# Kernel tuning notes

Hardware: AMD Instinct MI355X
Metric: run time of the kernel (lower is better)

The kernel has to match this reference:

```python
import jax, jax.numpy as jnp
import numpy as np

B, N, CS, CZ, CH, H, PQ, PV = 1, 768, 384, 128, 16, 12, 4, 8
INF, EPS, LN_EPS = 1e5, 1e-8, 1e-5


def setup_inputs() -> dict:
    key = jax.random.key(0)
    ks = jax.random.split(key, 16)
    def nrm(k, shape, scale=0.02):
        return jax.random.normal(k, shape, dtype=jnp.float32) * scale
    return {
        "s": jax.random.normal(ks[0], (B, N, CS), jnp.float32),
        "z": jax.random.normal(ks[1], (B, N, N, CZ), jnp.float32),
        "r_rot": jax.random.normal(ks[2], (B, N, 5, 3, 3), jnp.float32),
        "r_trans": jax.random.normal(ks[3], (B, N, 5, 3), jnp.float32),
        "mask": jnp.ones((B, N, 5), jnp.float32),
        "wq": nrm(ks[4], (H * CH, CS)), "bq": jnp.zeros((H * CH,), jnp.float32),
        "wkv": nrm(ks[5], (2 * H * CH, CS)), "bkv": jnp.zeros((2 * H * CH,), jnp.float32),
        "wqp": nrm(ks[6], (H * PQ * 3, CS)), "bqp": jnp.zeros((H * PQ * 3,), jnp.float32),
        "wkvp": nrm(ks[7], (H * (PQ + PV) * 3, CS)), "bkvp": jnp.zeros((H * (PQ + PV) * 3,), jnp.float32),
        "wb": nrm(ks[8], (H, CZ)), "bb": jnp.zeros((H,), jnp.float32),
        "head_w": nrm(ks[9], (H,), 0.5),
        "wout": nrm(ks[10], (CS, H * (CZ + CH + PV * 4))), "bout": jnp.zeros((CS,), jnp.float32),
        "wexp": nrm(ks[11], (5 * CS, CS)), "bexp": jnp.zeros((5 * CS,), jnp.float32),
        "ln_g": jnp.ones((CS,), jnp.float32), "ln_b": jnp.zeros((CS,), jnp.float32),
        "ww": nrm(ks[12], (1, CS)), "bw": jnp.zeros((1,), jnp.float32),
    }


def _mix(x, fg_mask, weight, ndims):
    # x: [B,N,5,...]; weighted blend of backbone frame (index 0) and mean of
    # masked functional-group frames (indices 1:5).
    bb_f = x[:, :, :1]
    m = fg_mask.reshape(fg_mask.shape + (1,) * ndims)
    fg = (x[:, :, 1:] * m).sum(axis=2, keepdims=True)
    denom = fg_mask.sum(-1, keepdims=True).reshape(fg_mask.shape[:2] + (1,) * (ndims + 1))
    fg = fg / (denom + 1e-8)
    w = weight.reshape(weight.shape[:2] + (1,) * (ndims + 1))
    return (w * bb_f + (1.0 - w) * fg)[:, :, 0]


def _ipa(s, z, r_rot, r_trans, mask, wq, bq, wkv, bkv, wqp, bqp, wkvp, bkvp,
         wb, bb, head_w, wout, bout, wexp, bexp, ln_g, ln_b, ww, bw):
    fg_mask = mask[..., 1:]            # [B,N,4]
    ulr = mask[..., 0]                 # [B,N]
    # softmax over a size-1 axis (as in original code -> all ones)
    weight = jax.nn.softmax(s @ ww.T + bw, axis=-1)   # [B,N,1]

    se = (s @ wexp.T + bexp).reshape(B, N, 5, CS)
    mu = se.mean(-1, keepdims=True)
    var = ((se - mu) ** 2).mean(-1, keepdims=True)
    se = (se - mu) * jax.lax.rsqrt(var + LN_EPS) * ln_g + ln_b

    q = _mix((se @ wq.T + bq).reshape(B, N, 5, H, CH), fg_mask, weight, 2)      # [B,N,H,CH]
    kv = _mix((se @ wkv.T + bkv).reshape(B, N, 5, H, 2 * CH), fg_mask, weight, 2)
    k, v = kv[..., :CH], kv[..., CH:]

    def pts_of(w_, b_, npts):
        lin = se @ w_.T + b_                                   # [B,N,5,3*H*npts]
        pts = jnp.moveaxis(lin.reshape(B, N, 5, 3, H * npts), -2, -1)  # [B,N,5,H*npts,3]
        pts = jnp.einsum('bnfij,bnfpj->bnfpi', r_rot, pts) + r_trans[:, :, :, None, :]
        return _mix(pts.reshape(B, N, 5, H, npts, 3), fg_mask, weight, 3)

    q_pts = pts_of(wqp, bqp, PQ)                               # [B,N,H,PQ,3]
    kv_pts = pts_of(wkvp, bkvp, PQ + PV)
    k_pts, v_pts = kv_pts[..., :PQ, :], kv_pts[..., PQ:, :]

    bias = z @ wb.T + bb                                       # [B,N,N,H]
    a = jnp.einsum('bihc,bjhc->bhij', q, k) * (1.0 / (3 * CH)) ** 0.5
    a = a + (1.0 / 3.0) ** 0.5 * jnp.transpose(bias, (0, 3, 1, 2))

    d2 = jnp.sum((q_pts[:, :, None] - k_pts[:, None]) ** 2, axis=-1)  # [B,N,N,H,PQ]
    hw = jax.nn.softplus(head_w) * (1.0 / (3 * (PQ * 9.0 / 2))) ** 0.5
    pt_att = -0.5 * jnp.sum(d2 * hw[:, None], axis=-1)         # [B,N,N,H]
    a = a + jnp.transpose(pt_att, (0, 3, 1, 2))
    sq_mask = INF * (ulr[:, :, None] * ulr[:, None, :] - 1.0)
    a = jax.nn.softmax(a + sq_mask[:, None], axis=-1)          # [B,H,N,N]

    o = jnp.einsum('bhij,bjhc->bihc', a, v).reshape(B, N, H * CH)
    o_pt = jnp.einsum('bhij,bjhpx->bihpx', a, v_pts)           # [B,N,H,PV,3]
    rot0, t0 = r_rot[:, :, 0], r_trans[:, :, 0]                # backbone frame
    # invert_apply: R^T (x - t)
    o_pt = jnp.einsum('bnik,bnhpi->bnhpk', rot0, o_pt - t0[:, :, None, None, :])
    o_pt_norm = jnp.sqrt(jnp.sum(o_pt ** 2, -1) + EPS).reshape(B, N, H * PV)
    o_pt = o_pt.reshape(B, N, H * PV, 3)
    o_pair = jnp.einsum('bhij,bijc->bihc', a, z).reshape(B, N, H * CZ)
    cat = jnp.concatenate([o, o_pt[..., 0], o_pt[..., 1], o_pt[..., 2], o_pt_norm, o_pair], -1)
    return cat @ wout.T + bout                                 # [B,N,CS]


def reference(s, z, r_rot, r_trans, mask, wq, bq, wkv, bkv, wqp, bqp, wkvp, bkvp,
              wb, bb, head_w, wout, bout, wexp, bexp, ln_g, ln_b, ww, bw):
    return _ipa(s, z, r_rot, r_trans, mask, wq, bq, wkv, bkv, wqp, bqp, wkvp, bkvp,
                wb, bb, head_w, wout, bout, wexp, bexp, ln_g, ln_b, ww, bw)
```

## Files before the change

### kernel.cpp

```cpp
#include <hip/hip_runtime.h>
#include <hip/hip_bf16.h>
#include <stdint.h>


typedef float  f32x4 __attribute__((ext_vector_type(4)));
typedef short  s16x8 __attribute__((ext_vector_type(8)));

__device__ __forceinline__ float bf2f(unsigned short u) {
    union { unsigned int i; float f; } v; v.i = ((unsigned int)u) << 16; return v.f;
}
__device__ __forceinline__ unsigned short f2bf(float f) {
    union { float f; unsigned int i; } v; v.f = f;
    unsigned int r = v.i + 0x7fffu + ((v.i >> 16) & 1u);
    return (unsigned short)(r >> 16);
}
__device__ __forceinline__ unsigned packbf2(float a, float b) {
    return (unsigned)f2bf(a) | ((unsigned)f2bf(b) << 16);
}
__device__ __forceinline__ float bval(int c,
    const float* bq, const float* bkv, const float* bqp, const float* bkvp)
{
    if (c < 192)      return bq[c];
    else if (c < 576) return bkv[c - 192];
    else if (c < 720) return bqp[c - 576];
    else              return bkvp[c - 720];
}

__global__ __launch_bounds__(256) void k_prep(
    const float* __restrict__ s, const float* __restrict__ wexp,
    const float* __restrict__ wq, const float* __restrict__ wkv,
    const float* __restrict__ wqp, const float* __restrict__ wkvp,
    const float* __restrict__ wout,
    const float* __restrict__ bq, const float* __restrict__ bkv,
    const float* __restrict__ bqp, const float* __restrict__ bkvp,
    unsigned short* __restrict__ s_bf, unsigned short* __restrict__ we_bf,
    unsigned short* __restrict__ wc_bf, unsigned short* __restrict__ wo_bf,
    float* __restrict__ bcat)
{
    const int x = blockIdx.x * 256 + threadIdx.x;
    if (x >= 1696896) return;
    if (x < 294912)            s_bf[x] = f2bf(s[x]);
    else if (x < 442368)       we_bf[x - 294912] = f2bf(wexp[x - 294912]);
    else if (x < 516096)       wc_bf[x - 442368] = f2bf(wq[x - 442368]);
    else if (x < 663552)       wc_bf[73728 + (x - 516096)] = f2bf(wkv[x - 516096]);
    else if (x < 718848)       wc_bf[221184 + (x - 663552)] = f2bf(wqp[x - 663552]);
    else if (x < 884736)       wc_bf[276480 + (x - 718848)] = f2bf(wkvp[x - 718848]);
    else if (x < 1695744)      wo_bf[x - 884736] = f2bf(wout[x - 884736]);
    else {
        int j = x - 1695744;
        bcat[j] = bval(j, bq, bkv, bqp, bkvp);
    }
}

__global__ __launch_bounds__(256) void k_mm(
    const unsigned short* __restrict__ A, int lda,
    const unsigned short* __restrict__ B, int ldb,
    float* __restrict__ C, int ldc, const float* __restrict__ bias,
    int nk, size_t pstride)
{
    const int m0 = blockIdx.x * 64, n0 = blockIdx.y * 64;
    const int koff = blockIdx.z * nk * 32;
    C += (size_t)blockIdx.z * pstride;
    const int t = threadIdx.x;
    const int lane = t & 63, wave = t >> 6, quad = lane >> 4, lcol = lane & 15;
    const int mh = (wave & 1) * 32, nh = (wave >> 1) * 32;
    __shared__ unsigned short As[64 * 40];
    __shared__ unsigned short Bs[64 * 40];
    const int lr = t >> 2, ls = (t & 3) * 8;
    const unsigned short* Ap = A + (size_t)(m0 + lr) * lda + koff + ls;
    const unsigned short* Bp = B + (size_t)(n0 + lr) * ldb + koff + ls;
    f32x4 acc[2][2] = {};

    uint4 av = *(const uint4*)Ap;
    uint4 bv = *(const uint4*)Bp;
    for (int kc = 0; kc < nk; ++kc) {
        __syncthreads();
        *(uint4*)&As[lr * 40 + ls] = av;
        *(uint4*)&Bs[lr * 40 + ls] = bv;
        __syncthreads();
        if (kc + 1 < nk) {
            av = *(const uint4*)(Ap + (size_t)(kc + 1) * 32);
            bv = *(const uint4*)(Bp + (size_t)(kc + 1) * 32);
        }
        s16x8 af0 = *(const s16x8*)&As[(mh + lcol) * 40 + quad * 8];
        s16x8 af1 = *(const s16x8*)&As[(mh + 16 + lcol) * 40 + quad * 8];
        s16x8 bf0 = *(const s16x8*)&Bs[(nh + lcol) * 40 + quad * 8];
        s16x8 bf1 = *(const s16x8*)&Bs[(nh + 16 + lcol) * 40 + quad * 8];
        acc[0][0] = __builtin_amdgcn_mfma_f32_16x16x32_bf16(af0, bf0, acc[0][0], 0, 0, 0);
        acc[0][1] = __builtin_amdgcn_mfma_f32_16x16x32_bf16(af0, bf1, acc[0][1], 0, 0, 0);
        acc[1][0] = __builtin_amdgcn_mfma_f32_16x16x32_bf16(af1, bf0, acc[1][0], 0, 0, 0);
        acc[1][1] = __builtin_amdgcn_mfma_f32_16x16x32_bf16(af1, bf1, acc[1][1], 0, 0, 0);
    }
    #pragma unroll
    for (int r = 0; r < 2; ++r)
        #pragma unroll
        for (int c = 0; c < 2; ++c) {
            int gn = n0 + nh + c * 16 + lcol;
            float bv2 = bias ? bias[gn] : 0.f;
            #pragma unroll
            for (int ii = 0; ii < 4; ++ii) {
                int gm = m0 + mh + r * 16 + quad * 4 + ii;
                C[(size_t)gm * ldc + gn] = acc[r][c][ii] + bv2;
            }
        }
}

__global__ __launch_bounds__(256) void k_ln(
    const float* __restrict__ se_raw, const float* __restrict__ ln_g,
    const float* __restrict__ ln_b, unsigned short* __restrict__ se0_bf)
{
    const int n = blockIdx.x * 4 + (threadIdx.x >> 6);
    const int lane = threadIdx.x & 63;
    const float* row = se_raw + (size_t)n * 384;
    float v[6], s1 = 0.f, s2 = 0.f;
    #pragma unroll
    for (int q = 0; q < 6; ++q) {
        v[q] = row[lane + q * 64];
        s1 += v[q]; s2 += v[q] * v[q];
    }
    for (int mk = 1; mk < 64; mk <<= 1) {
        s1 += __shfl_xor(s1, mk, 64);
        s2 += __shfl_xor(s2, mk, 64);
    }
    float mu = s1 * (1.f / 384.f);
    float var = s2 * (1.f / 384.f) - mu * mu;
    float rs = rsqrtf(fmaxf(var, 0.f) + 1e-5f);
    unsigned short* orow = se0_bf + (size_t)n * 384;
    #pragma unroll
    for (int q = 0; q < 6; ++q) {
        int c = lane + q * 64;
        orow[c] = f2bf((v[q] - mu) * rs * ln_g[c] + ln_b[c]);
    }
}

__global__ __launch_bounds__(256) void k_post(
    const float* __restrict__ lin,
    const float* __restrict__ r_rot, const float* __restrict__ r_trans,
    float* __restrict__ q_out, unsigned short* __restrict__ k_out,
    float* __restrict__ v_out, float* __restrict__ qp_out,
    unsigned short* __restrict__ kp_out, float* __restrict__ vp_out,
    float* __restrict__ k2_out)
{
    const int n0 = blockIdx.x * 8;
    const int t = threadIdx.x;
    __shared__ float kprot[8 * 144];

    for (int r = 0; r < 8; ++r) {
        const int n = n0 + r;
        const float* lrow = lin + (size_t)n * 1152;
        const float* rot = r_rot + (size_t)n * 45;
        for (int u = t; u < 1152; u += 256) {
            if (u < 192) {
                q_out[(size_t)n * 192 + u] = lrow[u];
            } else if (u < 576) {
                int l2 = u - 192, h = l2 >> 5, c = l2 & 31;
                float v = lrow[u];
                if (c < 16) k_out[(size_t)n * 192 + h * 16 + c] = f2bf(v);
                else        v_out[(size_t)n * 192 + h * 16 + (c - 16)] = v;
            } else {
                int y = u - 576;
                int pt = y / 3, i = y - pt * 3;
                float t0 = r_trans[(size_t)n * 15 + i];
                float v;
                if (pt < 48) {
                    v = rot[i*3+0] * lrow[576 + pt]
                      + rot[i*3+1] * lrow[576 + 48 + pt]
                      + rot[i*3+2] * lrow[576 + 96 + pt] + t0;
                    qp_out[(size_t)n * 144 + pt * 3 + i] = v;
                } else {
                    int pp = pt - 48;
                    v = rot[i*3+0] * lrow[720 + pp]
                      + rot[i*3+1] * lrow[720 + 144 + pp]
                      + rot[i*3+2] * lrow[720 + 288 + pp] + t0;
                    int h = pp / 12, pl = pp - h * 12;
                    if (pl < 4) {
                        kp_out[(size_t)n * 144 + (h * 4 + pl) * 3 + i] = f2bf(v);
                        kprot[r * 144 + (h * 4 + pl) * 3 + i] = v;
                    } else {
                        vp_out[(size_t)n * 288 + (h * 8 + (pl - 4)) * 3 + i] = v;
                    }
                }
            }
        }
    }
    __syncthreads();
    if (t < 96) {
        int r = t / 12, h = t - r * 12;
        float ss = 0.f;
        #pragma unroll
        for (int d = 0; d < 12; ++d) {
            float v = kprot[r * 144 + h * 12 + d];
            ss += v * v;
        }
        k2_out[(size_t)(n0 + r) * 12 + h] = ss;
    }
}

__global__ __launch_bounds__(256, 3) void k_attn(
    const float* __restrict__ z, const float* __restrict__ mask,
    const float* __restrict__ head_w, const float* __restrict__ wb,
    const float* __restrict__ bb,
    const float* __restrict__ r_rot, const float* __restrict__ r_trans,
    const float* __restrict__ q_ws, const float* __restrict__ qp_ws,
    const float* __restrict__ k2_ws,
    const unsigned short* __restrict__ k_bf, const float* __restrict__ v_f,
    const unsigned short* __restrict__ kp_bf, const float* __restrict__ vp_f,
    unsigned short* __restrict__ cat)
{
    const int i = blockIdx.x;
    const int t = threadIdx.x;
    const int lane = t & 63, wv = t >> 6;
    const int quad = lane >> 4, lcol = lane & 15;

    __shared__ short zb[2][64 * 136];
    __shared__ float L[64 * 17];
    __shared__ float Pt[16 * 68];
    __shared__ float qs[192], qps[144];
    __shared__ float ulra[768];
    __shared__ float m_s[16], l_s[16], alph_s[16], linv_s[16];
    __shared__ float optb[288];

    const float c_qk = 0.14433756729740643f;
    const float c_b  = 0.57735026918962576f;

    if (t < 192) qs[t]  = q_ws[(size_t)i * 192 + t];
    if (t < 144) qps[t] = qp_ws[(size_t)i * 144 + t];
    if (t >= 192 && t < 208) { int u = t - 192; m_s[u] = -1e30f; l_s[u] = 0.f; alph_s[u] = 1.f; }
    for (int x = t; x < 768; x += 256) ulra[x] = mask[(size_t)x * 5];
    for (int x = t; x < 4 * 68; x += 256) Pt[12 * 68 + x] = 0.f;
    const float ulr_i = mask[(size_t)i * 5];

    s16x8 wbf[4];
    #pragma unroll
    for (int kb = 0; kb < 4; ++kb) {
        #pragma unroll
        for (int j = 0; j < 8; ++j) {
            int c = kb * 32 + quad * 8 + j;
            wbf[kb][j] = (lcol < 12) ? (short)f2bf(wb[(size_t)lcol * 128 + c]) : (short)0;
        }
    }

    const int hh = (lcol < 12) ? lcol : 11;
    f32x4 qv[4], qpv[3];
    float q2_r = 0.f;
    {
        const float* qg  = q_ws  + (size_t)i * 192 + hh * 16;
        const float* qpg = qp_ws + (size_t)i * 144 + hh * 12;
        #pragma unroll
        for (int m = 0; m < 4; ++m) qv[m] = *(const f32x4*)(qg + m * 4);
        #pragma unroll
        for (int m = 0; m < 3; ++m) {
            qpv[m] = *(const f32x4*)(qpg + m * 4);
            #pragma unroll
            for (int e = 0; e < 4; ++e) q2_r += qpv[m][e] * qpv[m][e];
        }
    }
    float xh = head_w[hh];
    const float cpt_r = -0.5f * logf(1.f + __expf(xh)) * 0.13608276348795434f;
    const float cbb_r = c_b * bb[hh];

    f32x4 acc_op[2] = { {0.f,0.f,0.f,0.f}, {0.f,0.f,0.f,0.f} };
    f32x4 acc_s = {0.f,0.f,0.f,0.f};

    int vu = -1, vhalf = 0;
    if (t < 120) { vu = t; vhalf = 0; }
    else if (t >= 128 && t < 248) { vu = t - 128; vhalf = 1; }
    int vrole = -1; const float* vsrc = nullptr; int vstride = 0, voff = 0;
    if (vu >= 0) {
        if (vu < 48) { vrole = vu >> 2;       vsrc = v_f;  vstride = 192; voff = vu * 4; }
        else         { vrole = (vu - 48) / 6; vsrc = vp_f; vstride = 288; voff = (vu - 48) * 4; }
    }

    const int jlb = wv * 16 + quad * 4;
    const int zrow = wv * 16 + lcol;
    const int sigm = (zrow >> 3) & 3;

    const float* zbase = z + (size_t)i * 98304;
    f32x4 zr[8];
    #pragma unroll
    for (int sx = 0; sx < 8; ++sx)
        zr[sx] = *(const f32x4*)(zbase + (size_t)(t + sx * 256) * 4);
    #pragma unroll
    for (int sx = 0; sx < 8; ++sx) {
        int idx = t + sx * 256;
        int jl = idx >> 5, cq = idx & 31;
        int ch = (cq >> 1) ^ ((jl >> 3) & 3);
        uint2 pk;
        pk.x = packbf2(zr[sx][0], zr[sx][1]);
        pk.y = packbf2(zr[sx][2], zr[sx][3]);
        *(uint2*)&zb[0][jl * 136 + ch * 8 + (cq & 1) * 4] = pk;
    }
    #pragma unroll
    for (int sx = 0; sx < 8; ++sx)
        zr[sx] = *(const f32x4*)(zbase + 8192 + (size_t)(t + sx * 256) * 4);
    __syncthreads();

    int cur = 0;
    for (int tt = 0; tt < 12; ++tt) {
        const int j0 = tt * 64;

        uint4 ka[4], kb4[4]; uint2 p0[4], p1[4], p2[4]; float K2r[4];
        #pragma unroll
        for (int r = 0; r < 4; ++r) {
            int jr = j0 + jlb + r;
            const unsigned short* kr = k_bf + (size_t)jr * 192 + hh * 16;
            ka[r]  = *(const uint4*)kr;
            kb4[r] = *(const uint4*)(kr + 8);
            const unsigned short* pr = kp_bf + (size_t)jr * 144 + hh * 12;
            p0[r] = *(const uint2*)pr;
            p1[r] = *(const uint2*)(pr + 4);
            p2[r] = *(const uint2*)(pr + 8);
            K2r[r] = k2_ws[(size_t)jr * 12 + hh];
        }

        f32x4 d = {0.f, 0.f, 0.f, 0.f};
        #pragma unroll
        for (int kb = 0; kb < 4; ++kb) {
            s16x8 a = *(const s16x8*)&zb[cur][zrow * 136 + ((kb * 4 + quad) ^ sigm) * 8];
            d = __builtin_amdgcn_mfma_f32_16x16x32_bf16(a, wbf[kb], d, 0, 0, 0);
        }

        if (lcol < 12) {
            #pragma unroll
            for (int r = 0; r < 4; ++r) {
                int jl = jlb + r;
                const unsigned* kwa = (const unsigned*)&ka[r];
                const unsigned* kwb = (const unsigned*)&kb4[r];
                float qk = 0.f;
                #pragma unroll
                for (int m = 0; m < 4; ++m) {
                    qk += qv[m >> 1][(m & 1) * 2 + 0] * bf2f((unsigned short)(kwa[m] & 0xffffu));
                    qk += qv[m >> 1][(m & 1) * 2 + 1] * bf2f((unsigned short)(kwa[m] >> 16));
                }
                #pragma unroll
                for (int m = 0; m < 4; ++m) {
                    qk += qv[2 + (m >> 1)][(m & 1) * 2 + 0] * bf2f((unsigned short)(kwb[m] & 0xffffu));
                    qk += qv[2 + (m >> 1)][(m & 1) * 2 + 1] * bf2f((unsigned short)(kwb[m] >> 16));
                }
                float dp = 0.f;
                dp += qpv[0][0] * bf2f((unsigned short)(p0[r].x & 0xffffu));
                dp += qpv[0][1] * bf2f((unsigned short)(p0[r].x >> 16));
                dp += qpv[0][2] * bf2f((unsigned short)(p0[r].y & 0xffffu));
                dp += qpv[0][3] * bf2f((unsigned short)(p0[r].y >> 16));
                dp += qpv[1][0] * bf2f((unsigned short)(p1[r].x & 0xffffu));
                dp += qpv[1][1] * bf2f((unsigned short)(p1[r].x >> 16));
                dp += qpv[1][2] * bf2f((unsigned short)(p1[r].y & 0xffffu));
                dp += qpv[1][3] * bf2f((unsigned short)(p1[r].y >> 16));
                dp += qpv[2][0] * bf2f((unsigned short)(p2[r].x & 0xffffu));
                dp += qpv[2][1] * bf2f((unsigned short)(p2[r].x >> 16));
                dp += qpv[2][2] * bf2f((unsigned short)(p2[r].y & 0xffffu));
                dp += qpv[2][3] * bf2f((unsigned short)(p2[r].y >> 16));
                float ptt = cpt_r * (q2_r + K2r[r] - 2.f * dp);
                float lg = c_qk * qk + ptt + 1e5f * (ulr_i * ulra[j0 + jl] - 1.f)
                         + c_b * d[r] + cbb_r;
                L[jl * 17 + lcol] = lg;
            }
        }
        __syncthreads();

        if (t < 192) {
            int h = t >> 4, u = t & 15;
            float v0 = L[(u * 4 + 0) * 17 + h];
            float v1 = L[(u * 4 + 1) * 17 + h];
            float v2 = L[(u * 4 + 2) * 17 + h];
            float v3 = L[(u * 4 + 3) * 17 + h];
            float mx = fmaxf(fmaxf(v0, v1), fmaxf(v2, v3));
            for (int mk = 1; mk < 16; mk <<= 1) mx = fmaxf(mx, __shfl_xor(mx, mk, 16));
            float mold = m_s[h];
            float mnew = fmaxf(mold, mx);
            float w0 = __expf(v0 - mnew), w1 = __expf(v1 - mnew);
            float w2 = __expf(v2 - mnew), w3 = __expf(v3 - mnew);
            Pt[h * 68 + u * 4 + 0] = w0;
            Pt[h * 68 + u * 4 + 1] = w1;
            Pt[h * 68 + u * 4 + 2] = w2;
            Pt[h * 68 + u * 4 + 3] = w3;
            float sm = w0 + w1 + w2 + w3;
            for (int mk = 1; mk < 16; mk <<= 1) sm += __shfl_xor(sm, mk, 16);
            if (u == 0) {
                float al = __expf(mold - mnew);
                m_s[h] = mnew; alph_s[h] = al;
                l_s[h] = l_s[h] * al + sm;
            }
        }
        if (tt < 11) {
            #pragma unroll
            for (int sx = 0; sx < 8; ++sx) {
                int idx = t + sx * 256;
                int jl = idx >> 5, cq = idx & 31;
                int ch = (cq >> 1) ^ ((jl >> 3) & 3);
                uint2 pk;
                pk.x = packbf2(zr[sx][0], zr[sx][1]);
                pk.y = packbf2(zr[sx][2], zr[sx][3]);
                *(uint2*)&zb[cur ^ 1][jl * 136 + ch * 8 + (cq & 1) * 4] = pk;
            }
            if (tt < 10) {
                const float* znext = zbase + (size_t)(tt + 2) * 8192;
                #pragma unroll
                for (int sx = 0; sx < 8; ++sx)
                    zr[sx] = *(const f32x4*)(znext + (size_t)(t + sx * 256) * 4);
            }
        }
        __syncthreads();

        {
            float al[4];
            #pragma unroll
            for (int r = 0; r < 4; ++r) al[r] = alph_s[quad * 4 + r];
            #pragma unroll
            for (int nt = 0; nt < 2; ++nt)
                #pragma unroll
                for (int r = 0; r < 4; ++r) acc_op[nt][r] *= al[r];
            #pragma unroll
            for (int kb = 0; kb < 2; ++kb) {
                f32x4 pa = *(const f32x4*)&Pt[lcol * 68 + kb * 32 + quad * 8];
                f32x4 pb = *(const f32x4*)&Pt[lcol * 68 + kb * 32 + quad * 8 + 4];
                union { s16x8 v; unsigned u[4]; } af;
                af.u[0] = packbf2(pa[0], pa[1]);
                af.u[1] = packbf2(pa[2], pa[3]);
                af.u[2] = packbf2(pb[0], pb[1]);
                af.u[3] = packbf2(pb[2], pb[3]);
                #pragma unroll
                for (int nt = 0; nt < 2; ++nt) {
                    int c = wv * 32 + nt * 16 + lcol;
                    int csw = ((c >> 3) ^ quad) * 8 + (c & 7);
                    s16x8 bfg;
                    #pragma unroll
                    for (int j = 0; j < 8; ++j)
                        bfg[j] = zb[cur][(kb * 32 + quad * 8 + j) * 136 + csw];
                    acc_op[nt] = __builtin_amdgcn_mfma_f32_16x16x32_bf16(af.v, bfg, acc_op[nt], 0, 0, 0);
                }
            }
        }
        if (vu >= 0) {
            float alpha = alph_s[vrole];
            f32x4 a = acc_s;
            a[0] *= alpha; a[1] *= alpha; a[2] *= alpha; a[3] *= alpha;
            const float* prow = &Pt[vrole * 68 + vhalf * 32];
            const float* src = vsrc + (size_t)(j0 + vhalf * 32) * vstride + voff;
            #pragma unroll 4
            for (int jj = 0; jj < 32; jj += 4) {
                f32x4 p = *(const f32x4*)(prow + jj);
                #pragma unroll
                for (int m = 0; m < 4; ++m) {
                    f32x4 w = *(const f32x4*)(src + (size_t)(jj + m) * vstride);
                    float pm = p[m];
                    a[0] += pm * w[0];
                    a[1] += pm * w[1];
                    a[2] += pm * w[2];
                    a[3] += pm * w[3];
                }
            }
            acc_s = a;
        }
        if (tt < 11) cur ^= 1;
    }

    __syncthreads();
    if (t < 16) linv_s[t] = (t < 12) ? 1.f / l_s[t] : 0.f;
    float* vbuf = L;
    if (vu >= 0) {
        #pragma unroll
        for (int m = 0; m < 4; ++m) vbuf[(vu * 2 + vhalf) * 4 + m] = acc_s[m];
    }
    __syncthreads();
    unsigned short* crow = cat + (size_t)i * 2112;
    if (t < 120) {
        int role = (t < 48) ? (t >> 2) : (t - 48) / 6;
        float li = linv_s[role];
        float f[4];
        #pragma unroll
        for (int m = 0; m < 4; ++m)
            f[m] = (vbuf[(t * 2) * 4 + m] + vbuf[(t * 2 + 1) * 4 + m]) * li;
        if (t < 48) {
            #pragma unroll
            for (int m = 0; m < 4; ++m) crow[t * 4 + m] = f2bf(f[m]);
        } else {
            int e0 = (t - 48) * 4;
            optb[e0 + 0] = f[0]; optb[e0 + 1] = f[1];
            optb[e0 + 2] = f[2]; optb[e0 + 3] = f[3];
        }
    }
    {
        #pragma unroll
        for (int nt = 0; nt < 2; ++nt)
            #pragma unroll
            for (int r = 0; r < 4; ++r) {
                int h = quad * 4 + r;
                if (h < 12)
                    crow[576 + h * 128 + wv * 32 + nt * 16 + lcol] = f2bf(acc_op[nt][r] * linv_s[h]);
            }
    }
    __syncthreads();
    if (t < 96) {
        int hp = t;
        const float* rot = r_rot + (size_t)i * 45;
        float d0 = optb[hp * 3 + 0] - r_trans[(size_t)i * 15 + 0];
        float d1 = optb[hp * 3 + 1] - r_trans[(size_t)i * 15 + 1];
        float d2 = optb[hp * 3 + 2] - r_trans[(size_t)i * 15 + 2];
        float f0 = rot[0] * d0 + rot[3] * d1 + rot[6] * d2;
        float f1 = rot[1] * d0 + rot[4] * d1 + rot[7] * d2;
        float f2 = rot[2] * d0 + rot[5] * d1 + rot[8] * d2;
        crow[192 + hp] = f2bf(f0);
        crow[288 + hp] = f2bf(f1);
        crow[384 + hp] = f2bf(f2);
        crow[480 + hp] = f2bf(sqrtf(f0 * f0 + f1 * f1 + f2 * f2 + 1e-8f));
    }
}

__global__ __launch_bounds__(256) void k_out_red(
    const float* __restrict__ parts, const float* __restrict__ bout,
    float* __restrict__ out)
{
    const int x = blockIdx.x * 256 + threadIdx.x;
    float s = bout[x % 384];
    #pragma unroll
    for (int p = 0; p < 6; ++p) s += parts[(size_t)p * 294912 + x];
    out[x] = s;
}

extern "C" void kernel_launch(void* const* d_in, const int* in_sizes, int n_in,
                              void* d_out, int out_size, void* d_ws, size_t ws_size,
                              hipStream_t stream)
{
    const float* s       = (const float*)d_in[0];
    const float* z       = (const float*)d_in[1];
    const float* r_rot   = (const float*)d_in[2];
    const float* r_trans = (const float*)d_in[3];
    const float* mask    = (const float*)d_in[4];
    const float* wq      = (const float*)d_in[5];
    const float* bq      = (const float*)d_in[6];
    const float* wkv     = (const float*)d_in[7];
    const float* bkv     = (const float*)d_in[8];
    const float* wqp     = (const float*)d_in[9];
    const float* bqp     = (const float*)d_in[10];
    const float* wkvp    = (const float*)d_in[11];
    const float* bkvp    = (const float*)d_in[12];
    const float* wb      = (const float*)d_in[13];
    const float* bb      = (const float*)d_in[14];
    const float* head_w  = (const float*)d_in[15];
    const float* wout    = (const float*)d_in[16];
    const float* bout    = (const float*)d_in[17];
    const float* wexp    = (const float*)d_in[18];
    const float* bexp    = (const float*)d_in[19];
    const float* ln_g    = (const float*)d_in[20];
    const float* ln_b    = (const float*)d_in[21];

    float* wsf = (float*)d_ws;
    float* se_raw = wsf;
    float* lin    = wsf + 294912;
    float* qf     = wsf + 1179648;
    float* qpf    = wsf + 1327104;
    float* k2w    = wsf + 1437696;
    float* bcat   = wsf + 1446912;
    float* parts  = wsf + 1448064;
    float* vf     = wsf + 3217536;
    float* vpf    = wsf + 3364992;
    unsigned short* ub = (unsigned short*)(wsf + 3586176);
    unsigned short* s_bf   = ub;
    unsigned short* we_bf  = ub + 294912;
    unsigned short* wc_bf  = ub + 442368;
    unsigned short* wo_bf  = ub + 884736;
    unsigned short* se0_bf = ub + 1695744;
    unsigned short* kbf    = ub + 1990656;
    unsigned short* kpbf   = ub + 2138112;
    unsigned short* cat_bf = ub + 2248704;
    float* out = (float*)d_out;

    k_prep<<<6629, 256, 0, stream>>>(s, wexp, wq, wkv, wqp, wkvp, wout,
                                     bq, bkv, bqp, bkvp,
                                     s_bf, we_bf, wc_bf, wo_bf, bcat);
    k_mm<<<dim3(12, 6, 1), 256, 0, stream>>>(s_bf, 384, we_bf, 384,
                                             se_raw, 384, bexp, 12, 0);
    k_ln<<<192, 256, 0, stream>>>(se_raw, ln_g, ln_b, se0_bf);
    k_mm<<<dim3(12, 18, 1), 256, 0, stream>>>(se0_bf, 384, wc_bf, 384,
                                              lin, 1152, bcat, 12, 0);
    k_post<<<96, 256, 0, stream>>>(lin, r_rot, r_trans,
                                   qf, kbf, vf, qpf, kpbf, vpf, k2w);
    k_attn<<<768, 256, 0, stream>>>(z, mask, head_w, wb, bb, r_rot, r_trans,
                                    qf, qpf, k2w, kbf, vf, kpbf, vpf, cat_bf);
    k_mm<<<dim3(12, 6, 6), 256, 0, stream>>>(cat_bf, 2112, wo_bf, 2112,
                                             parts, 384, nullptr, 11, 294912);
    k_out_red<<<1152, 256, 0, stream>>>(parts, bout, out);
}
```

Before: 642.3 us.

## Split attention key range across two blocks per row and merge with new kernel

The attention kernel now launches two blocks per query row, each handling half of the key positions and writing unnormalised partial outputs plus running max and sum to a workspace. A new merge kernel rescales and combines the halves, normalises them, and applies the frame inverse transform before writing the bf16 concat row. The z tile double buffer in shared memory becomes a single buffer with an extra barrier per tile, and the occupancy hint in launch bounds is dropped. This doubles the grid of 768 blocks to spread work over more CUs, at the cost of an extra launch, a workspace round trip, and less overlap between z loading and compute.

```diff
diff --git a/kernel.cpp b/kernel.cpp
--- a/kernel.cpp
+++ b/kernel.cpp
@@ -196,29 +196,28 @@
     }
 }
 
-__global__ __launch_bounds__(256, 3) void k_attn(
+__global__ __launch_bounds__(256) void k_attn(
     const float* __restrict__ z, const float* __restrict__ mask,
     const float* __restrict__ head_w, const float* __restrict__ wb,
     const float* __restrict__ bb,
-    const float* __restrict__ r_rot, const float* __restrict__ r_trans,
     const float* __restrict__ q_ws, const float* __restrict__ qp_ws,
     const float* __restrict__ k2_ws,
     const unsigned short* __restrict__ k_bf, const float* __restrict__ v_f,
     const unsigned short* __restrict__ kp_bf, const float* __restrict__ vp_f,
-    unsigned short* __restrict__ cat)
-{
-    const int i = blockIdx.x;
+    float* __restrict__ parts)
+{
+    const int i = blockIdx.x >> 1;
+    const int half = blockIdx.x & 1;
     const int t = threadIdx.x;
     const int lane = t & 63, wv = t >> 6;
     const int quad = lane >> 4, lcol = lane & 15;
 
-    __shared__ short zb[2][64 * 136];
+    __shared__ short zb[64 * 136];
     __shared__ float L[64 * 17];
     __shared__ float Pt[16 * 68];
     __shared__ float qs[192], qps[144];
-    __shared__ float ulra[768];
-    __shared__ float m_s[16], l_s[16], alph_s[16], linv_s[16];
-    __shared__ float optb[288];
+    __shared__ float ulra[384];
+    __shared__ float m_s[16], l_s[16], alph_s[16];
 
     const float c_qk = 0.14433756729740643f;
     const float c_b  = 0.57735026918962576f;
@@ -226,7 +225,7 @@
     if (t < 192) qs[t]  = q_ws[(size_t)i * 192 + t];
     if (t < 144) qps[t] = qp_ws[(size_t)i * 144 + t];
     if (t >= 192 && t < 208) { int u = t - 192; m_s[u] = -1e30f; l_s[u] = 0.f; alph_s[u] = 1.f; }
-    for (int x = t; x < 768; x += 256) ulra[x] = mask[(size_t)x * 5];
+    for (int x = t; x < 384; x += 256) ulra[x] = mask[(size_t)(half * 384 + x) * 5];
     for (int x = t; x < 4 * 68; x += 256) Pt[12 * 68 + x] = 0.f;
     const float ulr_i = mask[(size_t)i * 5];
 
@@ -239,21 +238,18 @@
             wbf[kb][j] = (lcol < 12) ? (short)f2bf(wb[(size_t)lcol * 128 + c]) : (short)0;
         }
     }
+    __syncthreads();
 
     const int hh = (lcol < 12) ? lcol : 11;
     f32x4 qv[4], qpv[3];
     float q2_r = 0.f;
-    {
-        const float* qg  = q_ws  + (size_t)i * 192 + hh * 16;
-        const float* qpg = qp_ws + (size_t)i * 144 + hh * 12;
-        #pragma unroll
-        for (int m = 0; m < 4; ++m) qv[m] = *(const f32x4*)(qg + m * 4);
-        #pragma unroll
-        for (int m = 0; m < 3; ++m) {
-            qpv[m] = *(const f32x4*)(qpg + m * 4);
-            #pragma unroll
-            for (int e = 0; e < 4; ++e) q2_r += qpv[m][e] * qpv[m][e];
-        }
+    #pragma unroll
+    for (int m = 0; m < 4; ++m) qv[m] = *(const f32x4*)&qs[hh * 16 + m * 4];
+    #pragma unroll
+    for (int m = 0; m < 3; ++m) {
+        qpv[m] = *(const f32x4*)&qps[hh * 12 + m * 4];
+        #pragma unroll
+        for (int e = 0; e < 4; ++e) q2_r += qpv[m][e] * qpv[m][e];
     }
     float xh = head_w[hh];
     const float cpt_r = -0.5f * logf(1.f + __expf(xh)) * 0.13608276348795434f;
@@ -271,34 +267,39 @@
         else         { vrole = (vu - 48) / 6; vsrc = vp_f; vstride = 288; voff = (vu - 48) * 4; }
     }
 
+    const float* zbase = z + (size_t)i * 98304 + (size_t)half * 49152;
+    f32x4 zr[8];
+    #pragma unroll
+    for (int sx = 0; sx < 8; ++sx)
+        zr[sx] = *(const f32x4*)(zbase + (size_t)(t + sx * 256) * 4);
+
     const int jlb = wv * 16 + quad * 4;
     const int zrow = wv * 16 + lcol;
     const int sigm = (zrow >> 3) & 3;
 
-    const float* zbase = z + (size_t)i * 98304;
-    f32x4 zr[8];
-    #pragma unroll
-    for (int sx = 0; sx < 8; ++sx)
-        zr[sx] = *(const f32x4*)(zbase + (size_t)(t + sx * 256) * 4);
-    #pragma unroll
-    for (int sx = 0; sx < 8; ++sx) {
-        int idx = t + sx * 256;
-        int jl = idx >> 5, cq = idx & 31;
-        int ch = (cq >> 1) ^ ((jl >> 3) & 3);
-        uint2 pk;
-        pk.x = packbf2(zr[sx][0], zr[sx][1]);
-        pk.y = packbf2(zr[sx][2], zr[sx][3]);
-        *(uint2*)&zb[0][jl * 136 + ch * 8 + (cq & 1) * 4] = pk;
-    }
-    #pragma unroll
-    for (int sx = 0; sx < 8; ++sx)
-        zr[sx] = *(const f32x4*)(zbase + 8192 + (size_t)(t + sx * 256) * 4);
-    __syncthreads();
-
-    int cur = 0;
-    for (int tt = 0; tt < 12; ++tt) {
-        const int j0 = tt * 64;
-
+    for (int tt = 0; tt < 6; ++tt) {
+        const int j0 = half * 384 + tt * 64;
+        const int jloc0 = tt * 64;
+        __syncthreads();
+
+        #pragma unroll
+        for (int sx = 0; sx < 8; ++sx) {
+            int idx = t + sx * 256;
+            int jl = idx >> 5, cq = idx & 31;
+            int ch = (cq >> 1) ^ ((jl >> 3) & 3);
+            uint2 pk;
+            pk.x = packbf2(zr[sx][0], zr[sx][1]);
+            pk.y = packbf2(zr[sx][2], zr[sx][3]);
+            *(uint2*)&zb[jl * 136 + ch * 8 + (cq & 1) * 4] = pk;
+        }
+        __syncthreads();
+
+        if (tt < 5) {
+            const float* znext = zbase + (size_t)(tt + 1) * 8192;
+            #pragma unroll
+            for (int sx = 0; sx < 8; ++sx)
+                zr[sx] = *(const f32x4*)(znext + (size_t)(t + sx * 256) * 4);
+        }
         uint4 ka[4], kb4[4]; uint2 p0[4], p1[4], p2[4]; float K2r[4];
         #pragma unroll
         for (int r = 0; r < 4; ++r) {
@@ -316,7 +317,7 @@
         f32x4 d = {0.f, 0.f, 0.f, 0.f};
         #pragma unroll
         for (int kb = 0; kb < 4; ++kb) {
-            s16x8 a = *(const s16x8*)&zb[cur][zrow * 136 + ((kb * 4 + quad) ^ sigm) * 8];
+            s16x8 a = *(const s16x8*)&zb[zrow * 136 + ((kb * 4 + quad) ^ sigm) * 8];
             d = __builtin_amdgcn_mfma_f32_16x16x32_bf16(a, wbf[kb], d, 0, 0, 0);
         }
 
@@ -351,7 +352,7 @@
                 dp += qpv[2][2] * bf2f((unsigned short)(p2[r].y & 0xffffu));
                 dp += qpv[2][3] * bf2f((unsigned short)(p2[r].y >> 16));
                 float ptt = cpt_r * (q2_r + K2r[r] - 2.f * dp);
-                float lg = c_qk * qk + ptt + 1e5f * (ulr_i * ulra[j0 + jl] - 1.f)
+                float lg = c_qk * qk + ptt + 1e5f * (ulr_i * ulra[jloc0 + jl] - 1.f)
                          + c_b * d[r] + cbb_r;
                 L[jl * 17 + lcol] = lg;
             }
@@ -382,24 +383,6 @@
                 l_s[h] = l_s[h] * al + sm;
             }
         }
-        if (tt < 11) {
-            #pragma unroll
-            for (int sx = 0; sx < 8; ++sx) {
-                int idx = t + sx * 256;
-                int jl = idx >> 5, cq = idx & 31;
-                int ch = (cq >> 1) ^ ((jl >> 3) & 3);
-                uint2 pk;
-                pk.x = packbf2(zr[sx][0], zr[sx][1]);
-                pk.y = packbf2(zr[sx][2], zr[sx][3]);
-                *(uint2*)&zb[cur ^ 1][jl * 136 + ch * 8 + (cq & 1) * 4] = pk;
-            }
-            if (tt < 10) {
-                const float* znext = zbase + (size_t)(tt + 2) * 8192;
-                #pragma unroll
-                for (int sx = 0; sx < 8; ++sx)
-                    zr[sx] = *(const f32x4*)(znext + (size_t)(t + sx * 256) * 4);
-            }
-        }
         __syncthreads();
 
         {
@@ -426,7 +409,7 @@
                     s16x8 bfg;
                     #pragma unroll
                     for (int j = 0; j < 8; ++j)
-                        bfg[j] = zb[cur][(kb * 32 + quad * 8 + j) * 136 + csw];
+                        bfg[j] = zb[(kb * 32 + quad * 8 + j) * 136 + csw];
                     acc_op[nt] = __builtin_amdgcn_mfma_f32_16x16x32_bf16(af.v, bfg, acc_op[nt], 0, 0, 0);
                 }
             }
@@ -452,32 +435,29 @@
             }
             acc_s = a;
         }
-        if (tt < 11) cur ^= 1;
     }
 
     __syncthreads();
-    if (t < 16) linv_s[t] = (t < 12) ? 1.f / l_s[t] : 0.f;
+    float* pr = parts + (size_t)(i * 2 + half) * 2048;
+    if (t < 12) { pr[2016 + t] = m_s[t]; pr[2028 + t] = l_s[t]; }
     float* vbuf = L;
     if (vu >= 0) {
         #pragma unroll
         for (int m = 0; m < 4; ++m) vbuf[(vu * 2 + vhalf) * 4 + m] = acc_s[m];
     }
     __syncthreads();
-    unsigned short* crow = cat + (size_t)i * 2112;
     if (t < 120) {
-        int role = (t < 48) ? (t >> 2) : (t - 48) / 6;
-        float li = linv_s[role];
         float f[4];
         #pragma unroll
         for (int m = 0; m < 4; ++m)
-            f[m] = (vbuf[(t * 2) * 4 + m] + vbuf[(t * 2 + 1) * 4 + m]) * li;
+            f[m] = vbuf[(t * 2) * 4 + m] + vbuf[(t * 2 + 1) * 4 + m];
         if (t < 48) {
             #pragma unroll
-            for (int m = 0; m < 4; ++m) crow[t * 4 + m] = f2bf(f[m]);
+            for (int m = 0; m < 4; ++m) pr[t * 4 + m] = f[m];
         } else {
             int e0 = (t - 48) * 4;
-            optb[e0 + 0] = f[0]; optb[e0 + 1] = f[1];
-            optb[e0 + 2] = f[2]; optb[e0 + 3] = f[3];
+            pr[192 + e0 + 0] = f[0]; pr[192 + e0 + 1] = f[1];
+            pr[192 + e0 + 2] = f[2]; pr[192 + e0 + 3] = f[3];
         }
     }
     {
@@ -487,16 +467,50 @@
             for (int r = 0; r < 4; ++r) {
                 int h = quad * 4 + r;
                 if (h < 12)
-                    crow[576 + h * 128 + wv * 32 + nt * 16 + lcol] = f2bf(acc_op[nt][r] * linv_s[h]);
+                    pr[480 + h * 128 + wv * 32 + nt * 16 + lcol] = acc_op[nt][r];
             }
     }
+}
+
+__global__ __launch_bounds__(256) void k_merge(
+    const float* __restrict__ parts,
+    const float* __restrict__ r_rot, const float* __restrict__ r_trans,
+    unsigned short* __restrict__ cat)
+{
+    const int i = blockIdx.x;
+    const int t = threadIdx.x;
+    const float* p1 = parts + (size_t)(i * 2 + 0) * 2048;
+    const float* p2 = parts + (size_t)(i * 2 + 1) * 2048;
+    __shared__ float w1s[12], w2s[12], lis[12];
+    if (t < 12) {
+        float m1 = p1[2016 + t], l1 = p1[2028 + t];
+        float m2 = p2[2016 + t], l2 = p2[2028 + t];
+        float m = fmaxf(m1, m2);
+        float w1 = __expf(m1 - m), w2 = __expf(m2 - m);
+        w1s[t] = w1; w2s[t] = w2;
+        lis[t] = 1.f / (w1 * l1 + w2 * l2);
+    }
     __syncthreads();
+    unsigned short* crow = cat + (size_t)i * 2112;
+    if (t < 192) {
+        int h = t >> 4;
+        crow[t] = f2bf((w1s[h] * p1[t] + w2s[h] * p2[t]) * lis[h]);
+    }
+    #pragma unroll
+    for (int k = 0; k < 6; ++k) {
+        int c = t + k * 256;
+        int h = c >> 7;
+        crow[576 + c] = f2bf((w1s[h] * p1[480 + c] + w2s[h] * p2[480 + c]) * lis[h]);
+    }
     if (t < 96) {
-        int hp = t;
+        int hp = t, h = hp >> 3;
         const float* rot = r_rot + (size_t)i * 45;
-        float d0 = optb[hp * 3 + 0] - r_trans[(size_t)i * 15 + 0];
-        float d1 = optb[hp * 3 + 1] - r_trans[(size_t)i * 15 + 1];
-        float d2 = optb[hp * 3 + 2] - r_trans[(size_t)i * 15 + 2];
+        float o0 = (w1s[h] * p1[192 + hp * 3 + 0] + w2s[h] * p2[192 + hp * 3 + 0]) * lis[h];
+        float o1 = (w1s[h] * p1[192 + hp * 3 + 1] + w2s[h] * p2[192 + hp * 3 + 1]) * lis[h];
+        float o2 = (w1s[h] * p1[192 + hp * 3 + 2] + w2s[h] * p2[192 + hp * 3 + 2]) * lis[h];
+        float d0 = o0 - r_trans[(size_t)i * 15 + 0];
+        float d1 = o1 - r_trans[(size_t)i * 15 + 1];
+        float d2 = o2 - r_trans[(size_t)i * 15 + 2];
         float f0 = rot[0] * d0 + rot[3] * d1 + rot[6] * d2;
         float f1 = rot[1] * d0 + rot[4] * d1 + rot[7] * d2;
         float f2 = rot[2] * d0 + rot[5] * d1 + rot[8] * d2;
@@ -552,7 +566,7 @@
     float* qpf    = wsf + 1327104;
     float* k2w    = wsf + 1437696;
     float* bcat   = wsf + 1446912;
-    float* parts  = wsf + 1448064;
+    float* gparts = wsf + 1448064;
     float* vf     = wsf + 3217536;
     float* vpf    = wsf + 3364992;
     unsigned short* ub = (unsigned short*)(wsf + 3586176);
@@ -564,6 +578,7 @@
     unsigned short* kbf    = ub + 1990656;
     unsigned short* kpbf   = ub + 2138112;
     unsigned short* cat_bf = ub + 2248704;
+    float* pa_ws  = wsf + 5521536;
     float* out = (float*)d_out;
 
     k_prep<<<6629, 256, 0, stream>>>(s, wexp, wq, wkv, wqp, wkvp, wout,
@@ -576,9 +591,10 @@
                                               lin, 1152, bcat, 12, 0);
     k_post<<<96, 256, 0, stream>>>(lin, r_rot, r_trans,
                                    qf, kbf, vf, qpf, kpbf, vpf, k2w);
-    k_attn<<<768, 256, 0, stream>>>(z, mask, head_w, wb, bb, r_rot, r_trans,
-                                    qf, qpf, k2w, kbf, vf, kpbf, vpf, cat_bf);
+    k_attn<<<1536, 256, 0, stream>>>(z, mask, head_w, wb, bb,
+                                     qf, qpf, k2w, kbf, vf, kpbf, vpf, pa_ws);
+    k_merge<<<768, 256, 0, stream>>>(pa_ws, r_rot, r_trans, cat_bf);
     k_mm<<<dim3(12, 6, 6), 256, 0, stream>>>(cat_bf, 2112, wo_bf, 2112,
-                                             parts, 384, nullptr, 11, 294912);
-    k_out_red<<<1152, 256, 0, stream>>>(parts, bout, out);
-}
+                                             gparts, 384, nullptr, 11, 294912);
+    k_out_red<<<1152, 256, 0, stream>>>(gparts, bout, out);
+}
```

New measurement: 559.6 us. 1.15x faster.
